# Kernel tuning notes

Hardware: AMD Instinct MI355X
Metric: run time of the kernel (lower is better)

## Reference

```python
import jax, jax.numpy as jnp
import numpy as np

B, H, W, CIN = 4, 56, 56, 64
FILTERS, NDG, KS = 64, 4, 3
FIG = FILTERS // NDG  # filters per deformable group
K = KS * KS           # kernel taps
PAD = (KS - 1) // 2   # 'same' padding for stride 1, dilation 1


def setup_inputs() -> dict:
    key = jax.random.key(0)
    k1, k2, k3, k4 = jax.random.split(key, 4)
    x = jax.random.normal(k1, (B, H, W, CIN), jnp.float32)
    offset_kernel = jax.random.normal(k2, (KS, KS, CIN, K * NDG * 2), jnp.float32) * 0.01
    offset_bias = jax.random.normal(k3, (K * NDG * 2,), jnp.float32) * 0.1
    kernel = jax.random.normal(k4, (KS, KS, FILTERS, CIN), jnp.float32) * (1.0 / np.sqrt(K * CIN))
    return {"x": x, "offset_kernel": offset_kernel, "offset_bias": offset_bias, "kernel": kernel}


def reference(x, offset_kernel, offset_bias, kernel):
    # 1) offset prediction conv (SAME padding, stride 1, dilation 1)
    offset = jax.lax.conv_general_dilated(
        x, offset_kernel, window_strides=(1, 1), padding='SAME',
        dimension_numbers=('NHWC', 'HWIO', 'NHWC')) + offset_bias
    out_h, out_w = offset.shape[1], offset.shape[2]
    # 2) pad input exactly like the layer's _pad_input for 'same'
    xp = jnp.pad(x, ((0, 0), (PAD, PAD), (PAD, PAD), (0, 0)))
    in_h, in_w = xp.shape[1], xp.shape[2]
    # 3) offsets -> [B, oh, ow, K*NDG], channel order (tap k, group g)
    offset = offset.reshape(B, out_h, out_w, K * NDG, 2)
    y_off, x_off = offset[..., 0], offset[..., 1]
    # 4) base conv sampling grid in padded coords (stride=1, dilation=1)
    oh = jnp.arange(out_h)
    ow = jnp.arange(out_w)
    ki = jnp.arange(KS)
    kj = jnp.arange(KS)
    y_base = jnp.broadcast_to(oh[:, None, None, None] + ki[None, None, :, None],
                              (out_h, out_w, KS, KS)).reshape(out_h, out_w, K)
    x_base = jnp.broadcast_to(ow[None, :, None, None] + kj[None, None, None, :],
                              (out_h, out_w, KS, KS)).reshape(out_h, out_w, K)
    # tile over deformable groups: index layout k*NDG + g
    y_base = jnp.repeat(y_base, NDG, axis=-1).astype(jnp.float32)  # [oh,ow,K*NDG]
    x_base = jnp.repeat(x_base, NDG, axis=-1).astype(jnp.float32)
    y = jnp.clip(y_base[None] + y_off, 0.0, in_h - 1)
    xc = jnp.clip(x_base[None] + x_off, 0.0, in_w - 1)
    y0 = jnp.floor(y).astype(jnp.int32)
    x0 = jnp.floor(xc).astype(jnp.int32)
    y1 = jnp.clip(y0 + 1, 0, in_h - 1)
    x1 = jnp.clip(x1_ := x0 + 1, 0, in_w - 1)
    y0 = jnp.clip(y0, 0, in_h - 1)
    x0 = jnp.clip(x0, 0, in_w - 1)

    def gather(yy, xx):  # [B,oh,ow,K*NDG] int -> [B,oh,ow,K*NDG,CIN]
        return jax.vmap(lambda img, a, b: img[a, b])(xp, yy, xx)

    p0 = gather(y0, x0)
    p1 = gather(y0, x1)
    p2 = gather(y1, x0)
    p3 = gather(y1, x1)
    y0f, y1f = y0.astype(jnp.float32), y1.astype(jnp.float32)
    x0f, x1f = x0.astype(jnp.float32), x1.astype(jnp.float32)
    w0 = ((y1f - y) * (x1f - xc))[..., None]
    w1 = ((y1f - y) * (xc - x0f))[..., None]
    w2 = ((y - y0f) * (x1f - xc))[..., None]
    w3 = ((y - y0f) * (xc - x0f))[..., None]
    pixels = w0 * p0 + w1 * p1 + w2 * p2 + w3 * p3  # [B,oh,ow,K*NDG,CIN]
    pixels = pixels.reshape(B, out_h, out_w, KS, KS, NDG, CIN)
    # 5) grouped combination: filter f = g*FIG + r uses group g; sum over taps and Cin
    kW = kernel.reshape(KS, KS, NDG, FIG, CIN)
    out = jnp.einsum('bhwijgc,ijgfc->bhwgf', pixels, kW)
    return out.reshape(B, out_h, out_w, FILTERS)
```

## Files before the change

### kernel.cpp

```cpp
#include <hip/hip_runtime.h>


#define NH 56
#define NW 56
#define NC 64
#define NDG 4
#define NK 9
#define NOFF 72
#define NOFFP 80
#define NF 64
#define KTOT 576
#define HWPIX 3136
#define NPIX 12544

#define PW    14
#define WR    5
#define WC    18
#define WPOS  (WR * WC)
#define NBLK  (4 * NH * 4)

#define WS_OFFKT 0
#define WS_WK    92160

typedef _Float16 half8   __attribute__((ext_vector_type(8)));
typedef _Float16 half4   __attribute__((ext_vector_type(4)));
typedef float    floatx4 __attribute__((ext_vector_type(4)));

__global__ __launch_bounds__(256)
void dcn_prep(const float* __restrict__ offk,
              const float* __restrict__ wk,
              _Float16* __restrict__ offkt,
              _Float16* __restrict__ wkh)
{
    const int i = blockIdx.x * 256 + threadIdx.x;
    if (i < NOFFP * KTOT) {
        const int oc = i / KTOT;
        const int kk = i - oc * KTOT;
        const float v = (oc < NOFF) ? offk[kk * NOFF + oc] : 0.0f;
        offkt[i] = (_Float16)v;
    }
    const int j = i - NOFFP * KTOT;
    if (j >= 0 && j < NK * NF * NC) wkh[j] = (_Float16)wk[j];
}

__device__ __forceinline__ int winh_idx(int pos, int c) {
    return (pos << 6) + (c ^ ((pos & 7) << 3));
}

__global__ __launch_bounds__(256, 4)
void dcn_main(const float* __restrict__ x,
              const _Float16* __restrict__ offkt,
              const float* __restrict__ offb,
              const _Float16* __restrict__ wkh,
              float* __restrict__ out)
{
    __shared__ __align__(16) _Float16 s_winh[WPOS * NC];
    __shared__ float s_off[PW * NOFF];
    __shared__ __align__(16) float s_cww[36 * 16 * 4];
    __shared__ __align__(8)  unsigned s_cwl[36 * 16 * 2];

    const int tid  = threadIdx.x;
    const int w    = tid >> 6;
    const int lane = tid & 63;
    const int m    = lane & 15;
    const int kq   = lane >> 4;
    const int kq8  = kq * 8;

    const int blk = blockIdx.x;
    const int b   = blk / (NH * 4);
    const int r2  = blk - b * (NH * 4);
    const int oh  = r2 >> 2;
    const int ow0 = (r2 & 3) * PW;
    const int bb  = b * HWPIX;

    for (int i = tid; i < WPOS * 16; i += 256) {
        const int pos = i >> 4;
        const int g4  = (i & 15) * 4;
        const int ry  = pos / WC;
        const int rx  = pos - ry * WC;
        const int iy  = oh + ry - 2;
        const int ix  = ow0 + rx - 2;
        float4 v = make_float4(0.f, 0.f, 0.f, 0.f);
        if ((unsigned)iy < NH && (unsigned)ix < NW)
            v = *(const float4*)&x[(size_t)((bb + iy * NW + ix) * NC) + g4];
        half4 h;
        h[0] = (_Float16)v.x; h[1] = (_Float16)v.y;
        h[2] = (_Float16)v.z; h[3] = (_Float16)v.w;
        *(half4*)&s_winh[winh_idx(pos, g4)] = h;
    }
    __syncthreads();

    const int oc0 = w * 16 + m;
    floatx4 acc0, acc1;
    { const float bv = offb[oc0]; acc0 = (floatx4){bv, bv, bv, bv}; }
    { const float bv = (w == 3 && m < 8) ? offb[64 + m] : 0.0f;
      acc1 = (floatx4){bv, bv, bv, bv}; }

    #pragma unroll
    for (int k = 0; k < NK; ++k) {
        const int ki = k / 3, kj = k - 3 * ki;
        const int pos = (ki + 1) * WC + (m + kj + 1);
        #pragma unroll
        for (int s = 0; s < 2; ++s) {
            const half8 af = *(const half8*)&s_winh[winh_idx(pos, s * 32 + kq8)];
            const int kkb = k * 64 + s * 32 + kq8;
            const half8 bf0 = *(const half8*)&offkt[(size_t)oc0 * KTOT + kkb];
            acc0 = __builtin_amdgcn_mfma_f32_16x16x32_f16(af, bf0, acc0, 0, 0, 0);
            if (w == 3) {
                const half8 bf1 = *(const half8*)&offkt[(size_t)(64 + m) * KTOT + kkb];
                acc1 = __builtin_amdgcn_mfma_f32_16x16x32_f16(af, bf1, acc1, 0, 0, 0);
            }
        }
    }
    #pragma unroll
    for (int r = 0; r < 4; ++r)
        if (kq * 4 + r < PW)
            s_off[(kq * 4 + r) * NOFF + oc0] = acc0[r];
    if (w == 3 && m < 8) {
        #pragma unroll
        for (int r = 0; r < 4; ++r)
            if (kq * 4 + r < PW)
                s_off[(kq * 4 + r) * NOFF + 64 + m] = acc1[r];
    }
    __syncthreads();

    for (int i = tid; i < 36 * 16; i += 256) {
        const int kg = i >> 4;
        const int p  = i & 15;
        float4 wv = make_float4(0.f, 0.f, 0.f, 0.f);
        unsigned c0 = 0, c1 = 0;
        if (p < PW) {
            const int k  = kg >> 2;
            const int ki = k / 3, kj = k - 3 * ki;
            const int ow = ow0 + p;
            const float offy = s_off[p * NOFF + kg * 2 + 0];
            const float offx = s_off[p * NOFF + kg * 2 + 1];
            float yv = fminf(fmaxf((float)(oh + ki) + offy, 0.0f), 57.0f);
            float xv = fminf(fmaxf((float)(ow + kj) + offx, 0.0f), 57.0f);
            const float y0f = floorf(yv), x0f = floorf(xv);
            const int y0 = (int)y0f, x0 = (int)x0f;
            const int y1 = min(y0 + 1, 57), x1 = min(x0 + 1, 57);
            const float ly = yv - y0f,       lx = xv - x0f;
            const float hy = (float)y1 - yv, hx = (float)x1 - xv;
            const bool vy0 = (unsigned)(y0 - 1) < NH;
            const bool vy1 = (unsigned)(y1 - 1) < NH;
            const bool vx0 = (unsigned)(x0 - 1) < NW;
            const bool vx1 = (unsigned)(x1 - 1) < NW;
            wv = make_float4((vy0 && vx0) ? hy * hx : 0.0f,
                             (vy0 && vx1) ? hy * lx : 0.0f,
                             (vy1 && vx0) ? ly * hx : 0.0f,
                             (vy1 && vx1) ? ly * lx : 0.0f);
            const int y0c = min(max(y0 - 1, 0), NH - 1);
            const int y1c = min(max(y1 - 1, 0), NH - 1);
            const int x0c = min(max(x0 - 1, 0), NW - 1);
            const int x1c = min(max(x1 - 1, 0), NW - 1);
            const int ry0 = y0c - oh + 2, ry1 = y1c - oh + 2;
            const int rx0 = x0c - ow0 + 2, rx1 = x1c - ow0 + 2;
            if ((unsigned)ry0 < WR && (unsigned)ry1 < WR &&
                (unsigned)rx0 < WC && (unsigned)rx1 < WC) {
                c0 = (unsigned)(ry0 * WC + rx0) | ((unsigned)(ry0 * WC + rx1) << 16);
                c1 = (unsigned)(ry1 * WC + rx0) | ((unsigned)(ry1 * WC + rx1) << 16);
            } else {
                c0 = 0x80000000u | ((unsigned)y0c << 18) | ((unsigned)x0c << 12)
                   | ((unsigned)y1c << 6) | (unsigned)x1c;
                c1 = c0;
            }
        }
        *(float4*)&s_cww[i * 4] = wv;
        s_cwl[i * 2 + 0] = c0;
        s_cwl[i * 2 + 1] = c1;
    }
    __syncthreads();

    floatx4 accB = (floatx4){0.f, 0.f, 0.f, 0.f};
    const int tb = w * 16 + m;
    float4   cw = *(const float4*)&s_cww[tb * 4];
    unsigned c0 = s_cwl[tb * 2 + 0];
    unsigned c1 = s_cwl[tb * 2 + 1];
    #pragma unroll 1
    for (int k = 0; k < NK; ++k) {
        const int tn = (k + 1 < NK ? k + 1 : k) * 64 + tb;
        const float4   cwn = *(const float4*)&s_cww[tn * 4];
        const unsigned c0n = s_cwl[tn * 2 + 0];
        const unsigned c1n = s_cwl[tn * 2 + 1];

        const _Float16* wp = &wkh[(size_t)(k * NF + w * 16 + m) * NC];
        const half8 bf0 = *(const half8*)&wp[kq8];
        const half8 bf1 = *(const half8*)&wp[32 + kq8];

        half8 q00a, q01a, q10a, q11a;
        half8 q00b, q01b, q10b, q11b;
        if (__builtin_expect((c0 & 0x80000000u) == 0, 1)) {
            const int p00 = c0 & 0xFFFF, p01 = c0 >> 16;
            const int p10 = c1 & 0xFFFF, p11 = c1 >> 16;
            const int ca = kq8, cb = 32 + kq8;
            q00a = *(const half8*)&s_winh[winh_idx(p00, ca)];
            q01a = *(const half8*)&s_winh[winh_idx(p01, ca)];
            q10a = *(const half8*)&s_winh[winh_idx(p10, ca)];
            q11a = *(const half8*)&s_winh[winh_idx(p11, ca)];
            q00b = *(const half8*)&s_winh[winh_idx(p00, cb)];
            q01b = *(const half8*)&s_winh[winh_idx(p01, cb)];
            q10b = *(const half8*)&s_winh[winh_idx(p10, cb)];
            q11b = *(const half8*)&s_winh[winh_idx(p11, cb)];
        } else {
            const int y0c = (c0 >> 18) & 63, x0c = (c0 >> 12) & 63;
            const int y1c = (c0 >> 6) & 63,  x1c = c0 & 63;
            const int i00 = (bb + y0c * NW + x0c) * NC;
            const int i01 = (bb + y0c * NW + x1c) * NC;
            const int i10 = (bb + y1c * NW + x0c) * NC;
            const int i11 = (bb + y1c * NW + x1c) * NC;
            #pragma unroll
            for (int j = 0; j < 8; ++j) {
                q00a[j] = (_Float16)x[i00 + kq8 + j];
                q01a[j] = (_Float16)x[i01 + kq8 + j];
                q10a[j] = (_Float16)x[i10 + kq8 + j];
                q11a[j] = (_Float16)x[i11 + kq8 + j];
                q00b[j] = (_Float16)x[i00 + 32 + kq8 + j];
                q01b[j] = (_Float16)x[i01 + 32 + kq8 + j];
                q10b[j] = (_Float16)x[i10 + 32 + kq8 + j];
                q11b[j] = (_Float16)x[i11 + 32 + kq8 + j];
            }
        }

        half8 af0, af1;
        #pragma unroll
        for (int j = 0; j < 8; ++j) {
            float v0 = cw.x * (float)q00a[j];
            v0 = fmaf(cw.y, (float)q01a[j], v0);
            v0 = fmaf(cw.z, (float)q10a[j], v0);
            v0 = fmaf(cw.w, (float)q11a[j], v0);
            af0[j] = (_Float16)v0;
            float v1 = cw.x * (float)q00b[j];
            v1 = fmaf(cw.y, (float)q01b[j], v1);
            v1 = fmaf(cw.z, (float)q10b[j], v1);
            v1 = fmaf(cw.w, (float)q11b[j], v1);
            af1[j] = (_Float16)v1;
        }
        accB = __builtin_amdgcn_mfma_f32_16x16x32_f16(af0, bf0, accB, 0, 0, 0);
        accB = __builtin_amdgcn_mfma_f32_16x16x32_f16(af1, bf1, accB, 0, 0, 0);
        cw = cwn; c0 = c0n; c1 = c1n;
    }

    #pragma unroll
    for (int r = 0; r < 4; ++r) {
        const int row = kq * 4 + r;
        if (row < PW)
            out[(size_t)(bb + oh * NW + ow0 + row) * NF + w * 16 + m] = accB[r];
    }
}

extern "C" void kernel_launch(void* const* d_in, const int* in_sizes, int n_in,
                              void* d_out, int out_size, void* d_ws, size_t ws_size,
                              hipStream_t stream) {
    const float* xin  = (const float*)d_in[0];
    const float* offk = (const float*)d_in[1];
    const float* offb = (const float*)d_in[2];
    const float* wk   = (const float*)d_in[3];
    float* outp = (float*)d_out;

    _Float16* offkt = (_Float16*)((char*)d_ws + WS_OFFKT);
    _Float16* wkh   = (_Float16*)((char*)d_ws + WS_WK);

    dcn_prep<<<324, 256, 0, stream>>>(offk, wk, offkt, wkh);
    dcn_main<<<NBLK, 256, 0, stream>>>(xin, offkt, offb, wkh, outp);
}
```

Baseline: 86.68 us.

## Widen per-block tile to 28 output pixels with 512-thread blocks

Each block now covers 28 output columns instead of 14, using 8 waves (two pixel halves times four filter groups) and a wider 5x32 shared input window. The window halo is shared across more pixels, so redundant global loads of x and per-block setup are reduced, and the grid is halved to 448 blocks. The cost is more shared memory and larger blocks, which may lower occupancy, and fewer blocks to spread across the CUs.

```diff
diff --git a/kernel.cpp b/kernel.cpp
--- a/kernel.cpp
+++ b/kernel.cpp
@@ -13,11 +13,12 @@
 #define HWPIX 3136
 #define NPIX 12544
 
-#define PW    14
+#define PW    28
+#define PWH   14
 #define WR    5
-#define WC    18
+#define WC    32
 #define WPOS  (WR * WC)
-#define NBLK  (4 * NH * 4)
+#define NBLK  (4 * NH * 2)
 
 #define WS_OFFKT 0
 #define WS_WK    92160
@@ -47,7 +48,7 @@
     return (pos << 6) + (c ^ ((pos & 7) << 3));
 }
 
-__global__ __launch_bounds__(256, 4)
+__global__ __launch_bounds__(512, 4)
 void dcn_main(const float* __restrict__ x,
               const _Float16* __restrict__ offkt,
               const float* __restrict__ offb,
@@ -56,24 +57,26 @@
 {
     __shared__ __align__(16) _Float16 s_winh[WPOS * NC];
     __shared__ float s_off[PW * NOFF];
-    __shared__ __align__(16) float s_cww[36 * 16 * 4];
-    __shared__ __align__(8)  unsigned s_cwl[36 * 16 * 2];
+    __shared__ __align__(16) float s_cww[36 * 32 * 4];
+    __shared__ __align__(8)  unsigned s_cwl[36 * 32 * 2];
 
     const int tid  = threadIdx.x;
-    const int w    = tid >> 6;
+    const int wid  = tid >> 6;
+    const int g    = wid & 3;
+    const int mt   = wid >> 2;
     const int lane = tid & 63;
     const int m    = lane & 15;
     const int kq   = lane >> 4;
     const int kq8  = kq * 8;
 
     const int blk = blockIdx.x;
-    const int b   = blk / (NH * 4);
-    const int r2  = blk - b * (NH * 4);
-    const int oh  = r2 >> 2;
-    const int ow0 = (r2 & 3) * PW;
+    const int b   = blk / (NH * 2);
+    const int r2  = blk - b * (NH * 2);
+    const int oh  = r2 >> 1;
+    const int ow0 = (r2 & 1) * PW;
     const int bb  = b * HWPIX;
 
-    for (int i = tid; i < WPOS * 16; i += 256) {
+    for (int i = tid; i < WPOS * 16; i += 512) {
         const int pos = i >> 4;
         const int g4  = (i & 15) * 4;
         const int ry  = pos / WC;
@@ -90,43 +93,47 @@
     }
     __syncthreads();
 
-    const int oc0 = w * 16 + m;
+    const int oc0 = g * 16 + m;
     floatx4 acc0, acc1;
     { const float bv = offb[oc0]; acc0 = (floatx4){bv, bv, bv, bv}; }
-    { const float bv = (w == 3 && m < 8) ? offb[64 + m] : 0.0f;
+    { const float bv = (g == 3 && m < 8) ? offb[64 + m] : 0.0f;
       acc1 = (floatx4){bv, bv, bv, bv}; }
 
     #pragma unroll
     for (int k = 0; k < NK; ++k) {
         const int ki = k / 3, kj = k - 3 * ki;
-        const int pos = (ki + 1) * WC + (m + kj + 1);
+        const int pos = (ki + 1) * WC + (mt * PWH + m + kj + 1);
         #pragma unroll
         for (int s = 0; s < 2; ++s) {
             const half8 af = *(const half8*)&s_winh[winh_idx(pos, s * 32 + kq8)];
             const int kkb = k * 64 + s * 32 + kq8;
             const half8 bf0 = *(const half8*)&offkt[(size_t)oc0 * KTOT + kkb];
             acc0 = __builtin_amdgcn_mfma_f32_16x16x32_f16(af, bf0, acc0, 0, 0, 0);
-            if (w == 3) {
+            if (g == 3) {
                 const half8 bf1 = *(const half8*)&offkt[(size_t)(64 + m) * KTOT + kkb];
                 acc1 = __builtin_amdgcn_mfma_f32_16x16x32_f16(af, bf1, acc1, 0, 0, 0);
             }
         }
     }
     #pragma unroll
-    for (int r = 0; r < 4; ++r)
-        if (kq * 4 + r < PW)
-            s_off[(kq * 4 + r) * NOFF + oc0] = acc0[r];
-    if (w == 3 && m < 8) {
+    for (int r = 0; r < 4; ++r) {
+        const int row = kq * 4 + r;
+        if (row < PWH)
+            s_off[(mt * PWH + row) * NOFF + oc0] = acc0[r];
+    }
+    if (g == 3 && m < 8) {
         #pragma unroll
-        for (int r = 0; r < 4; ++r)
-            if (kq * 4 + r < PW)
-                s_off[(kq * 4 + r) * NOFF + 64 + m] = acc1[r];
+        for (int r = 0; r < 4; ++r) {
+            const int row = kq * 4 + r;
+            if (row < PWH)
+                s_off[(mt * PWH + row) * NOFF + 64 + m] = acc1[r];
+        }
     }
     __syncthreads();
 
-    for (int i = tid; i < 36 * 16; i += 256) {
-        const int kg = i >> 4;
-        const int p  = i & 15;
+    for (int i = tid; i < 36 * 32; i += 512) {
+        const int kg = i >> 5;
+        const int p  = i & 31;
         float4 wv = make_float4(0.f, 0.f, 0.f, 0.f);
         unsigned c0 = 0, c1 = 0;
         if (p < PW) {
@@ -173,18 +180,18 @@
     __syncthreads();
 
     floatx4 accB = (floatx4){0.f, 0.f, 0.f, 0.f};
-    const int tb = w * 16 + m;
+    const int tb = g * 32 + mt * PWH + m;
     float4   cw = *(const float4*)&s_cww[tb * 4];
     unsigned c0 = s_cwl[tb * 2 + 0];
     unsigned c1 = s_cwl[tb * 2 + 1];
     #pragma unroll 1
     for (int k = 0; k < NK; ++k) {
-        const int tn = (k + 1 < NK ? k + 1 : k) * 64 + tb;
+        const int tn = (k + 1 < NK ? k + 1 : k) * 128 + tb;
         const float4   cwn = *(const float4*)&s_cww[tn * 4];
         const unsigned c0n = s_cwl[tn * 2 + 0];
         const unsigned c1n = s_cwl[tn * 2 + 1];
 
-        const _Float16* wp = &wkh[(size_t)(k * NF + w * 16 + m) * NC];
+        const _Float16* wp = &wkh[(size_t)(k * NF + g * 16 + m) * NC];
         const half8 bf0 = *(const half8*)&wp[kq8];
         const half8 bf1 = *(const half8*)&wp[32 + kq8];
 
@@ -244,8 +251,9 @@
     #pragma unroll
     for (int r = 0; r < 4; ++r) {
         const int row = kq * 4 + r;
-        if (row < PW)
-            out[(size_t)(bb + oh * NW + ow0 + row) * NF + w * 16 + m] = accB[r];
+        if (row < PWH)
+            out[(size_t)(bb + oh * NW + ow0 + mt * PWH + row) * NF + g * 16 + m]
+                = accB[r];
     }
 }
 
@@ -262,5 +270,5 @@
     _Float16* wkh   = (_Float16*)((char*)d_ws + WS_WK);
 
     dcn_prep<<<324, 256, 0, stream>>>(offk, wk, offkt, wkh);
-    dcn_main<<<NBLK, 256, 0, stream>>>(xin, offkt, offb, wkh, outp);
-}
+    dcn_main<<<NBLK, 512, 0, stream>>>(xin, offkt, offb, wkh, outp);
+}
```

Result: no change. 86.77 us (+0.1%).

## Double block to 512 threads, split channel reduction across wave halves

Applied to the files above, without the earlier changes.

The main kernel now launches 512 threads per block. In the offset-conv stage, five waves each handle one 16-channel slice, which removes the extra MFMA chain that wave 3 used to run alone. In the deformable-sampling stage, each pair of waves splits the 64 input channels in half and the partial MFMA results are summed through a new shared reduction buffer. This gives more parallelism per output tile and shorter per-wave dependency chains, at the cost of an extra barrier, the shared-memory reduction and higher register pressure under the new launch bounds.

```diff
diff --git a/kernel.cpp b/kernel.cpp
--- a/kernel.cpp
+++ b/kernel.cpp
@@ -47,7 +47,7 @@
     return (pos << 6) + (c ^ ((pos & 7) << 3));
 }
 
-__global__ __launch_bounds__(256, 4)
+__global__ __launch_bounds__(512, 8)
 void dcn_main(const float* __restrict__ x,
               const _Float16* __restrict__ offkt,
               const float* __restrict__ offb,
@@ -58,9 +58,12 @@
     __shared__ float s_off[PW * NOFF];
     __shared__ __align__(16) float s_cww[36 * 16 * 4];
     __shared__ __align__(8)  unsigned s_cwl[36 * 16 * 2];
+    __shared__ __align__(16) float s_red[4 * 64 * 4];
 
     const int tid  = threadIdx.x;
-    const int w    = tid >> 6;
+    const int wid  = tid >> 6;
+    const int g    = wid & 3;
+    const int sh   = wid >> 2;
     const int lane = tid & 63;
     const int m    = lane & 15;
     const int kq   = lane >> 4;
@@ -73,7 +76,7 @@
     const int ow0 = (r2 & 3) * PW;
     const int bb  = b * HWPIX;
 
-    for (int i = tid; i < WPOS * 16; i += 256) {
+    for (int i = tid; i < WPOS * 16; i += 512) {
         const int pos = i >> 4;
         const int g4  = (i & 15) * 4;
         const int ry  = pos / WC;
@@ -90,41 +93,35 @@
     }
     __syncthreads();
 
-    const int oc0 = w * 16 + m;
-    floatx4 acc0, acc1;
-    { const float bv = offb[oc0]; acc0 = (floatx4){bv, bv, bv, bv}; }
-    { const float bv = (w == 3 && m < 8) ? offb[64 + m] : 0.0f;
-      acc1 = (floatx4){bv, bv, bv, bv}; }
-
-    #pragma unroll
-    for (int k = 0; k < NK; ++k) {
-        const int ki = k / 3, kj = k - 3 * ki;
-        const int pos = (ki + 1) * WC + (m + kj + 1);
+    if (wid < 5) {
+        const int oc0 = wid * 16 + m;
+        floatx4 acc;
+        { const float bv = (oc0 < NOFF) ? offb[oc0] : 0.0f;
+          acc = (floatx4){bv, bv, bv, bv}; }
         #pragma unroll
-        for (int s = 0; s < 2; ++s) {
-            const half8 af = *(const half8*)&s_winh[winh_idx(pos, s * 32 + kq8)];
-            const int kkb = k * 64 + s * 32 + kq8;
-            const half8 bf0 = *(const half8*)&offkt[(size_t)oc0 * KTOT + kkb];
-            acc0 = __builtin_amdgcn_mfma_f32_16x16x32_f16(af, bf0, acc0, 0, 0, 0);
-            if (w == 3) {
-                const half8 bf1 = *(const half8*)&offkt[(size_t)(64 + m) * KTOT + kkb];
-                acc1 = __builtin_amdgcn_mfma_f32_16x16x32_f16(af, bf1, acc1, 0, 0, 0);
-            }
-        }
-    }
-    #pragma unroll
-    for (int r = 0; r < 4; ++r)
-        if (kq * 4 + r < PW)
-            s_off[(kq * 4 + r) * NOFF + oc0] = acc0[r];
-    if (w == 3 && m < 8) {
-        #pragma unroll
-        for (int r = 0; r < 4; ++r)
-            if (kq * 4 + r < PW)
-                s_off[(kq * 4 + r) * NOFF + 64 + m] = acc1[r];
-    }
-    __syncthreads();
-
-    for (int i = tid; i < 36 * 16; i += 256) {
+        for (int k = 0; k < NK; ++k) {
+            const int ki = k / 3, kj = k - 3 * ki;
+            const int pos = (ki + 1) * WC + (m + kj + 1);
+            #pragma unroll
+            for (int s2 = 0; s2 < 2; ++s2) {
+                const half8 af = *(const half8*)&s_winh[winh_idx(pos, s2 * 32 + kq8)];
+                const int kkb = k * 64 + s2 * 32 + kq8;
+                const half8 bf = *(const half8*)&offkt[(size_t)oc0 * KTOT + kkb];
+                acc = __builtin_amdgcn_mfma_f32_16x16x32_f16(af, bf, acc, 0, 0, 0);
+            }
+        }
+        if (oc0 < NOFF) {
+            #pragma unroll
+            for (int r = 0; r < 4; ++r) {
+                const int row = kq * 4 + r;
+                if (row < PW)
+                    s_off[row * NOFF + oc0] = acc[r];
+            }
+        }
+    }
+    __syncthreads();
+
+    for (int i = tid; i < 36 * 16; i += 512) {
         const int kg = i >> 4;
         const int p  = i & 15;
         float4 wv = make_float4(0.f, 0.f, 0.f, 0.f);
@@ -173,7 +170,8 @@
     __syncthreads();
 
     floatx4 accB = (floatx4){0.f, 0.f, 0.f, 0.f};
-    const int tb = w * 16 + m;
+    const int sofs = sh * 32;
+    const int tb = g * 16 + m;
     float4   cw = *(const float4*)&s_cww[tb * 4];
     unsigned c0 = s_cwl[tb * 2 + 0];
     unsigned c1 = s_cwl[tb * 2 + 1];
@@ -184,68 +182,59 @@
         const unsigned c0n = s_cwl[tn * 2 + 0];
         const unsigned c1n = s_cwl[tn * 2 + 1];
 
-        const _Float16* wp = &wkh[(size_t)(k * NF + w * 16 + m) * NC];
-        const half8 bf0 = *(const half8*)&wp[kq8];
-        const half8 bf1 = *(const half8*)&wp[32 + kq8];
-
-        half8 q00a, q01a, q10a, q11a;
-        half8 q00b, q01b, q10b, q11b;
+        const half8 bf = *(const half8*)&wkh[(size_t)(k * NF + g * 16 + m) * NC +
+                                             sofs + kq8];
+
+        half8 q00, q01, q10, q11;
         if (__builtin_expect((c0 & 0x80000000u) == 0, 1)) {
             const int p00 = c0 & 0xFFFF, p01 = c0 >> 16;
             const int p10 = c1 & 0xFFFF, p11 = c1 >> 16;
-            const int ca = kq8, cb = 32 + kq8;
-            q00a = *(const half8*)&s_winh[winh_idx(p00, ca)];
-            q01a = *(const half8*)&s_winh[winh_idx(p01, ca)];
-            q10a = *(const half8*)&s_winh[winh_idx(p10, ca)];
-            q11a = *(const half8*)&s_winh[winh_idx(p11, ca)];
-            q00b = *(const half8*)&s_winh[winh_idx(p00, cb)];
-            q01b = *(const half8*)&s_winh[winh_idx(p01, cb)];
-            q10b = *(const half8*)&s_winh[winh_idx(p10, cb)];
-            q11b = *(const half8*)&s_winh[winh_idx(p11, cb)];
+            const int cc = sofs + kq8;
+            q00 = *(const half8*)&s_winh[winh_idx(p00, cc)];
+            q01 = *(const half8*)&s_winh[winh_idx(p01, cc)];
+            q10 = *(const half8*)&s_winh[winh_idx(p10, cc)];
+            q11 = *(const half8*)&s_winh[winh_idx(p11, cc)];
         } else {
             const int y0c = (c0 >> 18) & 63, x0c = (c0 >> 12) & 63;
             const int y1c = (c0 >> 6) & 63,  x1c = c0 & 63;
-            const int i00 = (bb + y0c * NW + x0c) * NC;
-            const int i01 = (bb + y0c * NW + x1c) * NC;
-            const int i10 = (bb + y1c * NW + x0c) * NC;
-            const int i11 = (bb + y1c * NW + x1c) * NC;
+            const int i00 = (bb + y0c * NW + x0c) * NC + sofs + kq8;
+            const int i01 = (bb + y0c * NW + x1c) * NC + sofs + kq8;
+            const int i10 = (bb + y1c * NW + x0c) * NC + sofs + kq8;
+            const int i11 = (bb + y1c * NW + x1c) * NC + sofs + kq8;
             #pragma unroll
             for (int j = 0; j < 8; ++j) {
-                q00a[j] = (_Float16)x[i00 + kq8 + j];
-                q01a[j] = (_Float16)x[i01 + kq8 + j];
-                q10a[j] = (_Float16)x[i10 + kq8 + j];
-                q11a[j] = (_Float16)x[i11 + kq8 + j];
-                q00b[j] = (_Float16)x[i00 + 32 + kq8 + j];
-                q01b[j] = (_Float16)x[i01 + 32 + kq8 + j];
-                q10b[j] = (_Float16)x[i10 + 32 + kq8 + j];
-                q11b[j] = (_Float16)x[i11 + 32 + kq8 + j];
-            }
-        }
-
-        half8 af0, af1;
+                q00[j] = (_Float16)x[i00 + j];
+                q01[j] = (_Float16)x[i01 + j];
+                q10[j] = (_Float16)x[i10 + j];
+                q11[j] = (_Float16)x[i11 + j];
+            }
+        }
+
+        half8 af;
         #pragma unroll
         for (int j = 0; j < 8; ++j) {
-            float v0 = cw.x * (float)q00a[j];
-            v0 = fmaf(cw.y, (float)q01a[j], v0);
-            v0 = fmaf(cw.z, (float)q10a[j], v0);
-            v0 = fmaf(cw.w, (float)q11a[j], v0);
-            af0[j] = (_Float16)v0;
-            float v1 = cw.x * (float)q00b[j];
-            v1 = fmaf(cw.y, (float)q01b[j], v1);
-            v1 = fmaf(cw.z, (float)q10b[j], v1);
-            v1 = fmaf(cw.w, (float)q11b[j], v1);
-            af1[j] = (_Float16)v1;
-        }
-        accB = __builtin_amdgcn_mfma_f32_16x16x32_f16(af0, bf0, accB, 0, 0, 0);
-        accB = __builtin_amdgcn_mfma_f32_16x16x32_f16(af1, bf1, accB, 0, 0, 0);
+            float v = cw.x * (float)q00[j];
+            v = fmaf(cw.y, (float)q01[j], v);
+            v = fmaf(cw.z, (float)q10[j], v);
+            v = fmaf(cw.w, (float)q11[j], v);
+            af[j] = (_Float16)v;
+        }
+        accB = __builtin_amdgcn_mfma_f32_16x16x32_f16(af, bf, accB, 0, 0, 0);
         cw = cwn; c0 = c0n; c1 = c1n;
     }
 
-    #pragma unroll
-    for (int r = 0; r < 4; ++r) {
-        const int row = kq * 4 + r;
-        if (row < PW)
-            out[(size_t)(bb + oh * NW + ow0 + row) * NF + w * 16 + m] = accB[r];
+    if (sh == 1)
+        *(floatx4*)&s_red[(g * 64 + lane) * 4] = accB;
+    __syncthreads();
+    if (sh == 0) {
+        const floatx4 o = *(const floatx4*)&s_red[(g * 64 + lane) * 4];
+        accB += o;
+        #pragma unroll
+        for (int r = 0; r < 4; ++r) {
+            const int row = kq * 4 + r;
+            if (row < PW)
+                out[(size_t)(bb + oh * NW + ow0 + row) * NF + g * 16 + m] = accB[r];
+        }
     }
 }
 
@@ -262,5 +251,5 @@
     _Float16* wkh   = (_Float16*)((char*)d_ws + WS_WK);
 
     dcn_prep<<<324, 256, 0, stream>>>(offk, wk, offkt, wkh);
-    dcn_main<<<NBLK, 256, 0, stream>>>(xin, offkt, offb, wkh, outp);
-}
+    dcn_main<<<NBLK, 512, 0, stream>>>(xin, offkt, offb, wkh, outp);
+}
```

After: 87.03 us. About the same (+0.4%).
